# Performance work log

Hardware: AMD Instinct MI355X
Metric: run time of the kernel (lower is better)

## Reference

```python
import jax, jax.numpy as jnp
import numpy as np

B, TOPK, E, C, K = 64, 2, 16, 1024, 4096


def setup_inputs() -> dict:
    key = jax.random.key(0)
    k1, k2, k3, k4, k5, k6 = jax.random.split(key, 6)
    return {
        "activated": jax.random.normal(k1, (B, TOPK, K), dtype=jnp.float32),
        "expert_indices": jax.random.randint(k2, (B, TOPK), 0, E, dtype=jnp.int64)
        if jax.config.jax_enable_x64 else jax.random.randint(k2, (B, TOPK), 0, E, dtype=jnp.int32),
        "expert_weights": jax.random.uniform(k3, (B, TOPK), dtype=jnp.float32),
        "mlp2_weight": jax.random.normal(k4, (E, C, K), dtype=jnp.float32),
        "mlp2_bias": jax.random.normal(k5, (E, C), dtype=jnp.float32),
        "residual_x": jax.random.normal(k6, (B, C), dtype=jnp.float32),
    }


def reference(activated, expert_indices, expert_weights, mlp2_weight, mlp2_bias, residual_x):
    # Gather per-token expert weights/biases: w [B, topk, C, K], b [B, topk, C]
    w = mlp2_weight[expert_indices]
    b = mlp2_bias[expert_indices]
    # Batched matvec per (token, expert slot): t [B, topk, C]
    t = jnp.einsum("beck,bek->bec", w, activated) + b
    # Weighted combine over top-k expert slots, plus residual: [B, C]
    return residual_x + jnp.einsum("bec,be->bc", t, expert_weights)
```

## Files before the change

kernel.cpp:

```cpp
#include <hip/hip_runtime.h>

#define BB    64
#define TOPK  2
#define EE    16
#define CC    1024
#define KK    4096

constexpr int RPB = 16;
constexpr int P   = 16;
constexpr int KS  = 8;
constexpr int KH  = KK / KS;
constexpr int NW  = KH / 4 / 64;

typedef float v4f __attribute__((ext_vector_type(4)));

__global__ __launch_bounds__(256, 4) void moe_mlp2(
    const float* __restrict__ act, const int* __restrict__ idx,
    const float* __restrict__ W, float* __restrict__ partial)
{
    __shared__ float sact[P][KH];
    __shared__ int   slist[BB * TOPK];
    __shared__ int   scnt;

    const int bid  = blockIdx.x;
    const int e    = bid >> 9;
    const int ct   = (bid >> 3) & 63;
    const int ks   = bid & (KS - 1);
    const int tid  = threadIdx.x;
    const int lane = tid & 63;
    const int wave = tid >> 6;
    const int row0 = ct * RPB + wave * 4;

    if (tid == 0) scnt = 0;
    __syncthreads();
    if (tid < BB * TOPK && idx[tid] == e) {
        int pos = atomicAdd(&scnt, 1);
        slist[pos] = tid;
    }
    __syncthreads();
    const int n = scnt;
    if (n == 0) return;

    const v4f* __restrict__ Wb =
        (const v4f*)(W + (size_t)(e * CC + row0) * KK + ks * KH);

    auto STAGE = [&](int g, int np) {
        for (int h = wave; h < 2 * np; h += 4) {
            int pr = slist[g + (h >> 1)];
            const float* gsrc = act + (size_t)pr * KK + ks * KH
                              + (h & 1) * (KH / 2) + lane * 4;
            __builtin_amdgcn_global_load_lds(
                (const __attribute__((address_space(1))) void*)gsrc,
                (__attribute__((address_space(3))) void*)
                    &sact[h >> 1][(h & 1) * (KH / 2)],
                16, 0, 0);
        }
    };

    v4f w[NW][4];
    {
        const int np0 = min(P, n);
        STAGE(0, np0);
        __builtin_amdgcn_sched_barrier(0);
#pragma unroll
        for (int kw = 0; kw < NW; kw++)
#pragma unroll
            for (int r = 0; r < 4; r++)
                w[kw][r] = __builtin_nontemporal_load(
                    Wb + (size_t)r * (KK / 4) + kw * 64 + lane);
        __builtin_amdgcn_sched_barrier(0);
        asm volatile("s_waitcnt vmcnt(8)" ::: "memory");
        __builtin_amdgcn_sched_barrier(0);
        __builtin_amdgcn_s_barrier();
        __builtin_amdgcn_sched_barrier(0);
    }

    for (int g = 0; g < n; g += P) {
        const int np = min(P, n - g);
        if (g) {
            __syncthreads();
            STAGE(g, np);
            __syncthreads();
        }

        float val[64];
#pragma unroll
        for (int i = 0; i < 64; i++) val[i] = 0.f;

#pragma unroll
        for (int kw = 0; kw < NW; kw++) {
            const int fb = (kw * 64 + lane) * 4;
#pragma unroll
            for (int pc = 0; pc < P / 4; pc++) {
                if (pc * 4 < np) {
#pragma unroll
                    for (int j = 0; j < 4; j++) {
                        const int p = pc * 4 + j;
                        const v4f a = *(const v4f*)&sact[p][fb];
#pragma unroll
                        for (int r = 0; r < 4; r++)
                            val[(p << 2) | r] +=
                                w[kw][r].x * a.x + w[kw][r].y * a.y +
                                w[kw][r].z * a.z + w[kw][r].w * a.w;
                    }
                }
            }
        }

        if (np <= 8) {
#pragma unroll
            for (int s = 0; s < 5; s++) {
                const int m = 1 << s;
                const bool hi = (lane & m) != 0;
#pragma unroll
                for (int i = 0; i < 32; i += 2 * m) {
                    float send = hi ? val[i] : val[i + m];
                    float recv = __shfl_xor(send, m, 64);
                    val[i] = (hi ? val[i + m] : val[i]) + recv;
                }
            }
            float v0 = val[0];
            v0 += __shfl_xor(v0, 32, 64);
            const int p = (lane & 31) >> 2;
            if (lane < 32 && p < np) {
                int pr = slist[g + p];
                partial[((size_t)pr * KS + ks) * CC + row0 + (lane & 3)] = v0;
            }
        } else {
#pragma unroll
            for (int s = 0; s < 6; s++) {
                const int m = 1 << s;
                const bool hi = (lane & m) != 0;
#pragma unroll
                for (int i = 0; i < 64; i += 2 * m) {
                    float send = hi ? val[i] : val[i + m];
                    float recv = __shfl_xor(send, m, 64);
                    val[i] = (hi ? val[i + m] : val[i]) + recv;
                }
            }
            const int p = lane >> 2;
            if (p < np) {
                int pr = slist[g + p];
                partial[((size_t)pr * KS + ks) * CC + row0 + (lane & 3)] =
                    val[0];
            }
        }
    }
}

__global__ __launch_bounds__(256) void finalize(
    const int* __restrict__ idx, const float* __restrict__ ew,
    const float* __restrict__ bias, const float* __restrict__ resid,
    const float* __restrict__ partial, float* __restrict__ out)
{
    const int i = blockIdx.x * 256 + threadIdx.x;
    const int b = i >> 10;
    const int c = i & (CC - 1);
    float v = resid[i];
#pragma unroll
    for (int s = 0; s < TOPK; s++) {
        const int pr = b * TOPK + s;
        const int e  = idx[pr];
        float t = bias[e * CC + c];
#pragma unroll
        for (int ks = 0; ks < KS; ks++)
            t += partial[((size_t)pr * KS + ks) * CC + c];
        v += ew[pr] * t;
    }
    out[i] = v;
}

extern "C" void kernel_launch(void* const* d_in, const int* in_sizes, int n_in,
                              void* d_out, int out_size, void* d_ws, size_t ws_size,
                              hipStream_t stream) {
    const float* act   = (const float*)d_in[0];
    const int*   idx   = (const int*)d_in[1];
    const float* ew    = (const float*)d_in[2];
    const float* W     = (const float*)d_in[3];
    const float* bias  = (const float*)d_in[4];
    const float* resid = (const float*)d_in[5];
    float* out = (float*)d_out;

    float* partial = (float*)d_ws;

    moe_mlp2<<<EE * 64 * KS, 256, 0, stream>>>(act, idx, W, partial);
    finalize<<<(BB * CC) / 256, 256, 0, stream>>>(
        idx, ew, bias, resid, partial, out);
}
```

Baseline: 351.5 us.

## Process two row tiles per block and halve token group size

New measurement: 488.4 us. 1.39x slower.

```diff
diff --git a/kernel.cpp b/kernel.cpp
--- a/kernel.cpp
+++ b/kernel.cpp
@@ -7,7 +7,8 @@
 #define KK    4096
 
 constexpr int RPB = 16;
-constexpr int P   = 16;
+constexpr int NCT = 2;
+constexpr int P   = 8;
 constexpr int KS  = 8;
 constexpr int KH  = KK / KS;
 constexpr int NW  = KH / 4 / 64;
@@ -23,13 +24,13 @@
     __shared__ int   scnt;
 
     const int bid  = blockIdx.x;
-    const int e    = bid >> 9;
-    const int ct   = (bid >> 3) & 63;
+    const int e    = bid >> 8;
+    const int ct2  = (bid >> 3) & 31;
     const int ks   = bid & (KS - 1);
     const int tid  = threadIdx.x;
     const int lane = tid & 63;
     const int wave = tid >> 6;
-    const int row0 = ct * RPB + wave * 4;
+    const int row0 = ct2 * (RPB * NCT) + wave * 4;
 
     if (tid == 0) scnt = 0;
     __syncthreads();
@@ -57,35 +58,30 @@
         }
     };
 
-    v4f w[NW][4];
+    v4f w[NCT][NW][4];
     {
         const int np0 = min(P, n);
         STAGE(0, np0);
         __builtin_amdgcn_sched_barrier(0);
 #pragma unroll
-        for (int kw = 0; kw < NW; kw++)
+        for (int t = 0; t < NCT; t++)
 #pragma unroll
-            for (int r = 0; r < 4; r++)
-                w[kw][r] = __builtin_nontemporal_load(
-                    Wb + (size_t)r * (KK / 4) + kw * 64 + lane);
+            for (int kw = 0; kw < NW; kw++)
+#pragma unroll
+                for (int r = 0; r < 4; r++)
+                    w[t][kw][r] = __builtin_nontemporal_load(
+                        Wb + ((size_t)t * RPB + r) * (KK / 4) + kw * 64 + lane);
         __builtin_amdgcn_sched_barrier(0);
-        asm volatile("s_waitcnt vmcnt(8)" ::: "memory");
+        asm volatile("s_waitcnt vmcnt(16)" ::: "memory");
         __builtin_amdgcn_sched_barrier(0);
         __builtin_amdgcn_s_barrier();
         __builtin_amdgcn_sched_barrier(0);
     }
 
-    for (int g = 0; g < n; g += P) {
-        const int np = min(P, n - g);
-        if (g) {
-            __syncthreads();
-            STAGE(g, np);
-            __syncthreads();
-        }
-
-        float val[64];
+    auto TILE = [&](const v4f (&wt)[NW][4], int row, int g, int np) {
+        float val[32];
 #pragma unroll
-        for (int i = 0; i < 64; i++) val[i] = 0.f;
+        for (int i = 0; i < 32; i++) val[i] = 0.f;
 
 #pragma unroll
         for (int kw = 0; kw < NW; kw++) {
@@ -100,51 +96,43 @@
 #pragma unroll
                         for (int r = 0; r < 4; r++)
                             val[(p << 2) | r] +=
-                                w[kw][r].x * a.x + w[kw][r].y * a.y +
-                                w[kw][r].z * a.z + w[kw][r].w * a.w;
+                                wt[kw][r].x * a.x + wt[kw][r].y * a.y +
+                                wt[kw][r].z * a.z + wt[kw][r].w * a.w;
                     }
                 }
             }
         }
 
-        if (np <= 8) {
 #pragma unroll
-            for (int s = 0; s < 5; s++) {
-                const int m = 1 << s;
-                const bool hi = (lane & m) != 0;
+        for (int s = 0; s < 5; s++) {
+            const int m = 1 << s;
+            const bool hi = (lane & m) != 0;
 #pragma unroll
-                for (int i = 0; i < 32; i += 2 * m) {
-                    float send = hi ? val[i] : val[i + m];
-                    float recv = __shfl_xor(send, m, 64);
-                    val[i] = (hi ? val[i + m] : val[i]) + recv;
-                }
-            }
-            float v0 = val[0];
-            v0 += __shfl_xor(v0, 32, 64);
-            const int p = (lane & 31) >> 2;
-            if (lane < 32 && p < np) {
-                int pr = slist[g + p];
-                partial[((size_t)pr * KS + ks) * CC + row0 + (lane & 3)] = v0;
-            }
-        } else {
-#pragma unroll
-            for (int s = 0; s < 6; s++) {
-                const int m = 1 << s;
-                const bool hi = (lane & m) != 0;
-#pragma unroll
-                for (int i = 0; i < 64; i += 2 * m) {
-                    float send = hi ? val[i] : val[i + m];
-                    float recv = __shfl_xor(send, m, 64);
-                    val[i] = (hi ? val[i + m] : val[i]) + recv;
-                }
-            }
-            const int p = lane >> 2;
-            if (p < np) {
-                int pr = slist[g + p];
-                partial[((size_t)pr * KS + ks) * CC + row0 + (lane & 3)] =
-                    val[0];
+            for (int i = 0; i < 32; i += 2 * m) {
+                float send = hi ? val[i] : val[i + m];
+                float recv = __shfl_xor(send, m, 64);
+                val[i] = (hi ? val[i + m] : val[i]) + recv;
             }
         }
+        float v0 = val[0];
+        v0 += __shfl_xor(v0, 32, 64);
+
+        const int p = (lane & 31) >> 2;
+        if (lane < 32 && p < np) {
+            int pr = slist[g + p];
+            partial[((size_t)pr * KS + ks) * CC + row + (lane & 3)] = v0;
+        }
+    };
+
+    for (int g = 0; g < n; g += P) {
+        const int np = min(P, n - g);
+        if (g) {
+            __syncthreads();
+            STAGE(g, np);
+            __syncthreads();
+        }
+        TILE(w[0], row0, g, np);
+        TILE(w[1], row0 + RPB, g, np);
     }
 }
 
@@ -183,7 +171,7 @@
 
     float* partial = (float*)d_ws;
 
-    moe_mlp2<<<EE * 64 * KS, 256, 0, stream>>>(act, idx, W, partial);
+    moe_mlp2<<<EE * 32 * KS, 256, 0, stream>>>(act, idx, W, partial);
     finalize<<<(BB * CC) / 256, 256, 0, stream>>>(
         idx, ew, bias, resid, partial, out);
 }
```
